# Kernel tuning notes

Measured on AMD Instinct MI355X. Metric: run time of the kernel, lower is better.

The kernel has to match this reference:

```python
import jax, jax.numpy as jnp
import numpy as np

NEG_SLOPE = 0.2


def setup_inputs() -> dict:
    key = jax.random.key(0)
    ks = jax.random.split(key, 7)
    N, E, IN, H, D = 100000, 1000000, 256, 4, 32
    feat = jax.random.normal(ks[0], (N, IN), dtype=jnp.float32)
    W_fc = jax.random.normal(ks[1], (H * D, IN), dtype=jnp.float32) * (1.0 / np.sqrt(IN))
    attn_l = jax.random.normal(ks[2], (1, H, D), dtype=jnp.float32) * 0.1
    attn_r = jax.random.normal(ks[3], (1, H, D), dtype=jnp.float32) * 0.1
    bias = jnp.zeros((H * D,), dtype=jnp.float32)
    src = jax.random.randint(ks[4], (E,), 0, N, dtype=jnp.int32)
    dst = jax.random.randint(ks[5], (E,), 0, N, dtype=jnp.int32)
    return {"feat": feat, "W_fc": W_fc, "attn_l": attn_l, "attn_r": attn_r, "bias": bias, "src": src, "dst": dst}


def reference(feat, W_fc, attn_l, attn_r, bias, src, dst):
    N = feat.shape[0]
    H, D = attn_l.shape[1], attn_l.shape[2]
    # fc projection; note: in the non-tuple path the module uses self.fc for
    # BOTH feat_src and feat_src2, so they are identical.
    h = (feat @ W_fc.T).reshape(N, H, D)  # [N,H,D]
    el = jnp.sum(h * attn_l, axis=-1)  # [N,H]
    er = jnpp_sum = jnp.sum(h * attn_r, axis=-1)  # [N,H]
    e = jax.nn.leaky_relu(el[src] + er[dst], NEG_SLOPE)  # [E,H]
    # edge softmax normalized over incoming edges of each dst node
    e_max = jax.ops.segment_max(e, dst, num_segments=N)  # [N,H]
    ex = jnp.exp(e - e_max[dst])
    denom = jax.ops.segment_sum(ex, dst, num_segments=N)  # [N,H]
    a = ex / denom[dst]  # [E,H]
    # attention-weighted aggregation: sum_e a_e * h[src_e] -> dst
    initial_ft = jax.ops.segment_sum(h[src] * a[:, :, None], dst, num_segments=N)
    # second path: u_mul_v then sum to dst (feat_src2 == feat_dst2 == h)
    add_ft = jax.ops.segment_sum(h[src] * h[dst], dst, num_segments=N)
    rst = initial_ft + add_ft + bias.reshape(1, H, D)
    return rst
```

## Files before the change

kernel.cpp:

```cpp
#include <hip/hip_runtime.h>
#include <hip/hip_bf16.h>
#include <hip/hip_fp16.h>
#include <math.h>

#define NEG_SLOPE 0.2f

typedef __attribute__((ext_vector_type(8))) short short8v;
typedef __attribute__((ext_vector_type(4))) float f32x4;

__device__ __forceinline__ float uas(unsigned int u) { return __uint_as_float(u); }

__device__ __forceinline__ unsigned short f2bf(float x) {
    __hip_bfloat16 b = __float2bfloat16(x);
    return *(unsigned short*)&b;
}

#define NPB_SHIFT 8
#define BIN_EDGES 2048
#define GEMM_EPT  4
#define BS_EPT    4
#define GEMM_BLOCKS 512

__global__ void k_prep(const float* __restrict__ W, const float* __restrict__ al,
                       const float* __restrict__ ar, short* __restrict__ wfrag,
                       int* __restrict__ bcount, int NB, int* __restrict__ tilectr) {
    int p = blockIdx.x * 256 + threadIdx.x;
    if (p < NB) bcount[p] = 0;
    if (p == 0) *tilectr = 0;
    if (p >= 144 * 32) return;
    int n = p >> 5, kg = p & 31;
    float v[8];
    if (n < 128) {
        const float* wp = W + (size_t)n * 256 + kg * 8;
        float4 v0 = *(const float4*)wp;
        float4 v1 = *(const float4*)(wp + 4);
        v[0] = v0.x; v[1] = v0.y; v[2] = v0.z; v[3] = v0.w;
        v[4] = v1.x; v[5] = v1.y; v[6] = v1.z; v[7] = v1.w;
    } else if (n < 136) {
        int i = n - 128, hh = i & 3, lr = i >> 2;
        const float* av = lr ? ar : al;
#pragma unroll
        for (int j = 0; j < 8; j++) v[j] = 0.f;
        for (int c = 0; c < 32; c++) {
            float a = av[hh * 32 + c];
            const float* wp = W + (size_t)(hh * 32 + c) * 256 + kg * 8;
#pragma unroll
            for (int j = 0; j < 8; j++) v[j] += a * wp[j];
        }
    } else {
#pragma unroll
        for (int j = 0; j < 8; j++) v[j] = 0.f;
    }
    short s8[8];
#pragma unroll
    for (int j = 0; j < 8; j++) s8[j] = (short)f2bf(v[j]);
    int kstep = kg >> 2, ntile = n >> 4;
    int L     = (kg & 3) * 16 + (n & 15);
    int slot  = kstep * 9 + ntile;
    *(short8v*)&wfrag[(slot * 64 + L) * 8] = *(short8v*)s8;
}

__global__ __launch_bounds__(512, 4) void k_gemm(const float* __restrict__ feat,
                                                 const short* __restrict__ wfrag,
                                                 unsigned short* __restrict__ hb,
                                                 float* __restrict__ el,
                                                 float* __restrict__ er, int N,
                                                 int ntiles,
                                                 int* __restrict__ tilectr,
                                                 const int* __restrict__ dst,
                                                 int* __restrict__ bcount,
                                                 int E, int NB) {
    __shared__ short wlds[36864];
    __shared__ int bh[512];
    __shared__ int tsh;
    const int t    = threadIdx.x;
    const int lane = t & 63;
    const int wave = t >> 6;
    const int g    = lane >> 4;
    const int c    = lane & 15;

#pragma unroll
    for (int i = 0; i < 9; i++) {
        int p = t + i * 512;
        *(short8v*)&wlds[(size_t)p * 8] = *(const short8v*)&wfrag[(size_t)p * 8];
    }
    __syncthreads();

    for (;;) {
        if (t == 0) tsh = atomicAdd(tilectr, 1);
        __syncthreads();
        const int tile = tsh;
        __syncthreads();
        if (tile >= ntiles) break;

        const int n0  = tile * 128;
        const int row = n0 + wave * 16 + c;
        const int rc  = row < N ? row : N - 1;
        const float* ap = feat + (size_t)rc * 256 + g * 8;

        float4 a4[16];
#pragma unroll
        for (int ks = 0; ks < 8; ks++) {
            a4[2 * ks]     = *(const float4*)(ap + ks * 32);
            a4[2 * ks + 1] = *(const float4*)(ap + ks * 32 + 4);
        }

        f32x4 acc[9];
#pragma unroll
        for (int nt = 0; nt < 9; nt++) acc[nt] = (f32x4){0.f, 0.f, 0.f, 0.f};

#pragma unroll
        for (int ks = 0; ks < 8; ks++) {
            float4 v0 = a4[2 * ks], v1 = a4[2 * ks + 1];
            short s8[8];
            s8[0] = (short)f2bf(v0.x); s8[1] = (short)f2bf(v0.y);
            s8[2] = (short)f2bf(v0.z); s8[3] = (short)f2bf(v0.w);
            s8[4] = (short)f2bf(v1.x); s8[5] = (short)f2bf(v1.y);
            s8[6] = (short)f2bf(v1.z); s8[7] = (short)f2bf(v1.w);
            short8v afrag = *(short8v*)s8;
#pragma unroll
            for (int nt = 0; nt < 9; nt++) {
                short8v b = *(short8v*)&wlds[(((size_t)ks * 9 + nt) * 64 + lane) * 8];
                acc[nt] = __builtin_amdgcn_mfma_f32_16x16x32_bf16(afrag, b, acc[nt], 0, 0, 0);
            }
        }

#pragma unroll
        for (int r = 0; r < 4; r++) {
            int m = n0 + wave * 16 + g * 4 + r;
            if (m < N) {
#pragma unroll
                for (int nt = 0; nt < 8; nt++)
                    hb[(size_t)m * 128 + nt * 16 + c] = f2bf(acc[nt][r]);
                float av = acc[8][r];
                if (c < 4)      el[(size_t)m * 4 + c]       = av;
                else if (c < 8) er[(size_t)m * 4 + (c - 4)] = av;
            }
        }
    }

    if ((size_t)blockIdx.x * BIN_EDGES < (size_t)E) {
        if (t < 512) bh[t] = 0;
        __syncthreads();
        int base = blockIdx.x * BIN_EDGES + t;
#pragma unroll
        for (int k = 0; k < GEMM_EPT; k++) {
            int idx = base + k * 512;
            if (idx < E) atomicAdd(&bh[dst[idx] >> NPB_SHIFT], 1);
        }
        __syncthreads();
        for (int i = t; i < NB; i += 512) {
            int h = bh[i];
            if (h) atomicAdd(&bcount[i], h);
        }
    }
}

__global__ __launch_bounds__(512) void k_bscan(const int* __restrict__ bcount,
                                               int* __restrict__ bbase,
                                               int* __restrict__ bcur,
                                               int* __restrict__ startA,
                                               int NB, int N) {
    __shared__ int s[512];
    int t = threadIdx.x;
    int h = (t < NB) ? bcount[t] : 0;
    s[t] = h;
    __syncthreads();
    for (int off = 1; off < 512; off <<= 1) {
        int v = (t >= off) ? s[t - off] : 0;
        __syncthreads();
        s[t] += v;
        __syncthreads();
    }
    int excl = s[t] - h;
    if (t <= NB) bbase[t] = excl;
    if (t < NB)  bcur[t]  = excl;
    if (t == 0)  startA[N] = s[511];
}

__global__ __launch_bounds__(512) void k_binscatter(const int* __restrict__ src,
                                                    const int* __restrict__ dst,
                                                    int* __restrict__ bcur,
                                                    unsigned int* __restrict__ binned,
                                                    int E, int NB) {
    __shared__ int hist[512];
    __shared__ int scn[512];
    __shared__ int lcur[512];
    __shared__ int gdelta[512];
    __shared__ int ebuf[BIN_EDGES];
    __shared__ int dbuf[BIN_EDGES];
    int t = threadIdx.x;
    hist[t] = 0;
    __syncthreads();
    int wbase = blockIdx.x * BIN_EDGES;
    int base  = wbase + t;
    int ne    = E - wbase; if (ne > BIN_EDGES) ne = BIN_EDGES;
    int sv[BS_EPT], dv[BS_EPT];
#pragma unroll
    for (int k = 0; k < BS_EPT; k++) {
        int idx = base + k * 512;
        if (idx < E) {
            sv[k] = src[idx];
            dv[k] = dst[idx];
            atomicAdd(&hist[dv[k] >> NPB_SHIFT], 1);
        } else {
            dv[k] = -1;
        }
    }
    __syncthreads();
    scn[t] = hist[t];
    __syncthreads();
    for (int off = 1; off < 512; off <<= 1) {
        int v = (t >= off) ? scn[t - off] : 0;
        __syncthreads();
        scn[t] += v;
        __syncthreads();
    }
    if (t < NB) {
        int h  = hist[t];
        int lb = scn[t] - h;
        int g  = h ? atomicAdd(&bcur[t], h) : 0;
        gdelta[t] = g - lb;
        lcur[t]   = lb;
    }
    __syncthreads();
#pragma unroll
    for (int k = 0; k < BS_EPT; k++) {
        if (dv[k] >= 0) {
            int bkt  = dv[k] >> NPB_SHIFT;
            int slot = atomicAdd(&lcur[bkt], 1);
            ebuf[slot] = sv[k];
            dbuf[slot] = dv[k];
        }
    }
    __syncthreads();
    for (int j = t; j < ne; j += 512) {
        int d = dbuf[j];
        binned[j + gdelta[d >> NPB_SHIFT]] =
            (unsigned int)ebuf[j] | ((unsigned int)(d & 255) << 24);
    }
}

__global__ __launch_bounds__(512) void k_csr(const unsigned int* __restrict__ binned,
                                             const int* __restrict__ bbase,
                                             int* __restrict__ startA,
                                             int* __restrict__ src_csr, int N) {
    __shared__ int hist[256];
    __shared__ int scn[256];
    __shared__ int cur[256];
    __shared__ int sbuf[4096];
    int b = blockIdx.x;
    int t = threadIdx.x;
    int base = bbase[b];
    int cnt  = bbase[b + 1] - base;
    int node0 = b << NPB_SHIFT;
    if (t < 256) hist[t] = 0;
    __syncthreads();
    for (int i = t; i < cnt; i += 512) {
        unsigned int e = binned[base + i];
        atomicAdd(&hist[e >> 24], 1);
    }
    __syncthreads();
    int h = (t < 256) ? hist[t] : 0;
    if (t < 256) scn[t] = h;
    __syncthreads();
    for (int off = 1; off < 256; off <<= 1) {
        int v = (t < 256 && t >= off) ? scn[t - off] : 0;
        __syncthreads();
        if (t < 256) scn[t] += v;
        __syncthreads();
    }
    if (t < 256) {
        int excl  = scn[t] - h;
        int gnode = node0 + t;
        if (gnode < N) startA[gnode] = base + excl;
        cur[t] = excl;
    }
    __syncthreads();
    if (cnt <= 4096) {
        for (int i = t; i < cnt; i += 512) {
            unsigned int e = binned[base + i];
            int p = atomicAdd(&cur[e >> 24], 1);
            sbuf[p] = (int)(e & 0xFFFFFFu);
        }
        __syncthreads();
        for (int i = t; i < cnt; i += 512)
            src_csr[base + i] = sbuf[i];
    } else {
        for (int i = t; i < cnt; i += 512) {
            unsigned int e = binned[base + i];
            int p = atomicAdd(&cur[e >> 24], 1);
            src_csr[base + p] = (int)(e & 0xFFFFFFu);
        }
    }
}

__global__ __launch_bounds__(256) void k_agg(
        const unsigned int* __restrict__ hbu,
        const float* __restrict__ el, const float* __restrict__ er,
        const int* __restrict__ src_csr, const int* __restrict__ start,
        const float* __restrict__ bias, float* __restrict__ out, int N) {
    int wid  = blockIdx.x * 4 + (threadIdx.x >> 6);
    int lane = threadIdx.x & 63;
    if (wid >= N) return;
    int beg = __builtin_amdgcn_readfirstlane(start[wid]);
    int end = __builtin_amdgcn_readfirstlane(start[wid + 1]);
    int dg  = end - beg;
    int head = lane >> 4;

    float er_own = er[(size_t)wid * 4 + head];
    unsigned int uh = hbu[(size_t)wid * 64 + lane];
    float2 bv = ((const float2*)bias)[lane];

    float S1x = 0.f, S1y = 0.f, S2x = 0.f, S2y = 0.f, dd = 0.f;
    int i = 0;
    for (; i + 8 <= dg; i += 8) {
        int b = beg + i;
        int s[8];
#pragma unroll
        for (int k = 0; k < 8; k++) s[k] = src_csr[b + k];
        unsigned int u[8];
#pragma unroll
        for (int k = 0; k < 8; k++) u[k] = hbu[(size_t)s[k] * 64 + lane];
        float ev[8];
#pragma unroll
        for (int k = 0; k < 8; k++) ev[k] = el[(size_t)s[k] * 4 + head];
#pragma unroll
        for (int k = 0; k < 8; k++) {
            float tt = ev[k] + er_own;
            tt = fmaxf(tt, NEG_SLOPE * tt);
            float w = __expf(tt);
            float x = uas(u[k] << 16), y = uas(u[k] & 0xFFFF0000u);
            S1x += x; S1y += y;
            S2x += w * x; S2y += w * y;
            dd  += w;
        }
    }
    for (; i + 4 <= dg; i += 4) {
        int b = beg + i;
        int s[4];
#pragma unroll
        for (int k = 0; k < 4; k++) s[k] = src_csr[b + k];
        unsigned int u[4];
#pragma unroll
        for (int k = 0; k < 4; k++) u[k] = hbu[(size_t)s[k] * 64 + lane];
        float ev[4];
#pragma unroll
        for (int k = 0; k < 4; k++) ev[k] = el[(size_t)s[k] * 4 + head];
#pragma unroll
        for (int k = 0; k < 4; k++) {
            float tt = ev[k] + er_own;
            tt = fmaxf(tt, NEG_SLOPE * tt);
            float w = __expf(tt);
            float x = uas(u[k] << 16), y = uas(u[k] & 0xFFFF0000u);
            S1x += x; S1y += y;
            S2x += w * x; S2y += w * y;
            dd  += w;
        }
    }
    for (; i < dg; i++) {
        int s0 = src_csr[beg + i];
        unsigned int u0 = hbu[(size_t)s0 * 64 + lane];
        float tt = el[(size_t)s0 * 4 + head] + er_own;
        tt = fmaxf(tt, NEG_SLOPE * tt);
        float w0 = __expf(tt);
        float x0 = uas(u0 << 16), y0 = uas(u0 & 0xFFFF0000u);
        S1x += x0; S1y += y0;
        S2x += w0 * x0; S2y += w0 * y0;
        dd  += w0;
    }

    float hvx = uas(uh << 16), hvy = uas(uh & 0xFFFF0000u);
    float inv = dd > 0.f ? 1.f / dd : 0.f;
    float ox = bv.x + hvx * S1x + S2x * inv;
    float oy = bv.y + hvy * S1y + S2y * inv;
    float2 o = {ox, oy};
    ((float2*)(out + (size_t)wid * 128))[lane] = o;
}

extern "C" void kernel_launch(void* const* d_in, const int* in_sizes, int n_in,
                              void* d_out, int out_size, void* d_ws, size_t ws_size,
                              hipStream_t stream) {
    const float* feat = (const float*)d_in[0];
    const float* W_fc = (const float*)d_in[1];
    const float* al   = (const float*)d_in[2];
    const float* ar   = (const float*)d_in[3];
    const float* bias = (const float*)d_in[4];
    const int*   src  = (const int*)d_in[5];
    const int*   dst  = (const int*)d_in[6];
    const int N = in_sizes[0] / 256;
    const int E = in_sizes[5];
    const int NB = (N + 255) >> NPB_SHIFT;

    char* ws = (char*)d_ws;
    size_t off = 0;
    unsigned int* hbu = (unsigned int*)(ws + off); off += (size_t)N * 64 * 4;
    float* el         = (float*)(ws + off); off += (size_t)N * 4 * 4;
    float* er         = (float*)(ws + off); off += (size_t)N * 4 * 4;
    int* startA       = (int*)(ws + off);   off += (size_t)(N + 1) * 4;
    int* src_csr      = (int*)(ws + off);   off += (size_t)E * 4;
    unsigned int* binned = (unsigned int*)(ws + off); off += (size_t)E * 4;
    short* wfrag      = (short*)(ws + off); off += (size_t)72 * 64 * 8 * 2;
    int* bcount       = (int*)(ws + off);   off += 2048;
    int* bbase        = (int*)(ws + off);   off += 2064;
    int* bcur         = (int*)(ws + off);   off += 2048;
    int* tilectr      = (int*)(ws + off);   off += 256;

    float* out = (float*)d_out;

    int ntiles = (N + 127) / 128;
    int binWG  = (E + BIN_EDGES - 1) / BIN_EDGES;
    int gemmWG = GEMM_BLOCKS > binWG ? GEMM_BLOCKS : binWG;

    k_prep<<<18, 256, 0, stream>>>(W_fc, al, ar, wfrag, bcount, NB, tilectr);
    k_gemm<<<gemmWG, 512, 0, stream>>>(feat, wfrag, (unsigned short*)hbu,
                                       el, er, N, ntiles, tilectr, dst, bcount,
                                       E, NB);
    k_bscan<<<1, 512, 0, stream>>>(bcount, bbase, bcur, startA, NB, N);
    k_binscatter<<<binWG, 512, 0, stream>>>(src, dst, bcur, binned, E, NB);
    k_csr<<<NB, 512, 0, stream>>>(binned, bbase, startA, src_csr, N);
    k_agg<<<(N + 3) / 4, 256, 0, stream>>>(hbu, el, er, src_csr, startA,
                                           bias, out, N);
}
```

Measured before the change: 272.0 us.

## Replace exact bucket counting and scan with fixed-capacity bucket slots

```diff
diff --git a/kernel.cpp b/kernel.cpp
--- a/kernel.cpp
+++ b/kernel.cpp
@@ -16,16 +16,17 @@
 }
 
 #define NPB_SHIFT 8
+#define BCAP_SHIFT 13
+#define BCAP (1 << BCAP_SHIFT)
 #define BIN_EDGES 2048
-#define GEMM_EPT  4
 #define BS_EPT    4
 #define GEMM_BLOCKS 512
 
 __global__ void k_prep(const float* __restrict__ W, const float* __restrict__ al,
                        const float* __restrict__ ar, short* __restrict__ wfrag,
-                       int* __restrict__ bcount, int NB, int* __restrict__ tilectr) {
+                       int* __restrict__ bcur, int NB, int* __restrict__ tilectr) {
     int p = blockIdx.x * 256 + threadIdx.x;
-    if (p < NB) bcount[p] = 0;
+    if (p < NB) bcur[p] = p << BCAP_SHIFT;
     if (p == 0) *tilectr = 0;
     if (p >= 144 * 32) return;
     int n = p >> 5, kg = p & 31;
@@ -66,12 +67,8 @@
                                                  float* __restrict__ el,
                                                  float* __restrict__ er, int N,
                                                  int ntiles,
-                                                 int* __restrict__ tilectr,
-                                                 const int* __restrict__ dst,
-                                                 int* __restrict__ bcount,
-                                                 int E, int NB) {
+                                                 int* __restrict__ tilectr) {
     __shared__ short wlds[36864];
-    __shared__ int bh[512];
     __shared__ int tsh;
     const int t    = threadIdx.x;
     const int lane = t & 63;
@@ -138,44 +135,6 @@
             }
         }
     }
-
-    if ((size_t)blockIdx.x * BIN_EDGES < (size_t)E) {
-        if (t < 512) bh[t] = 0;
-        __syncthreads();
-        int base = blockIdx.x * BIN_EDGES + t;
-#pragma unroll
-        for (int k = 0; k < GEMM_EPT; k++) {
-            int idx = base + k * 512;
-            if (idx < E) atomicAdd(&bh[dst[idx] >> NPB_SHIFT], 1);
-        }
-        __syncthreads();
-        for (int i = t; i < NB; i += 512) {
-            int h = bh[i];
-            if (h) atomicAdd(&bcount[i], h);
-        }
-    }
-}
-
-__global__ __launch_bounds__(512) void k_bscan(const int* __restrict__ bcount,
-                                               int* __restrict__ bbase,
-                                               int* __restrict__ bcur,
-                                               int* __restrict__ startA,
-                                               int NB, int N) {
-    __shared__ int s[512];
-    int t = threadIdx.x;
-    int h = (t < NB) ? bcount[t] : 0;
-    s[t] = h;
-    __syncthreads();
-    for (int off = 1; off < 512; off <<= 1) {
-        int v = (t >= off) ? s[t - off] : 0;
-        __syncthreads();
-        s[t] += v;
-        __syncthreads();
-    }
-    int excl = s[t] - h;
-    if (t <= NB) bbase[t] = excl;
-    if (t < NB)  bcur[t]  = excl;
-    if (t == 0)  startA[N] = s[511];
 }
 
 __global__ __launch_bounds__(512) void k_binscatter(const int* __restrict__ src,
@@ -242,8 +201,9 @@
 }
 
 __global__ __launch_bounds__(512) void k_csr(const unsigned int* __restrict__ binned,
-                                             const int* __restrict__ bbase,
+                                             const int* __restrict__ bcur,
                                              int* __restrict__ startA,
+                                             int* __restrict__ deg,
                                              int* __restrict__ src_csr, int N) {
     __shared__ int hist[256];
     __shared__ int scn[256];
@@ -251,8 +211,8 @@
     __shared__ int sbuf[4096];
     int b = blockIdx.x;
     int t = threadIdx.x;
-    int base = bbase[b];
-    int cnt  = bbase[b + 1] - base;
+    int base = b << BCAP_SHIFT;
+    int cnt  = bcur[b] - base;
     int node0 = b << NPB_SHIFT;
     if (t < 256) hist[t] = 0;
     __syncthreads();
@@ -273,7 +233,7 @@
     if (t < 256) {
         int excl  = scn[t] - h;
         int gnode = node0 + t;
-        if (gnode < N) startA[gnode] = base + excl;
+        if (gnode < N) { startA[gnode] = base + excl; deg[gnode] = h; }
         cur[t] = excl;
     }
     __syncthreads();
@@ -299,13 +259,13 @@
         const unsigned int* __restrict__ hbu,
         const float* __restrict__ el, const float* __restrict__ er,
         const int* __restrict__ src_csr, const int* __restrict__ start,
+        const int* __restrict__ deg,
         const float* __restrict__ bias, float* __restrict__ out, int N) {
     int wid  = blockIdx.x * 4 + (threadIdx.x >> 6);
     int lane = threadIdx.x & 63;
     if (wid >= N) return;
     int beg = __builtin_amdgcn_readfirstlane(start[wid]);
-    int end = __builtin_amdgcn_readfirstlane(start[wid + 1]);
-    int dg  = end - beg;
+    int dg  = __builtin_amdgcn_readfirstlane(deg[wid]);
     int head = lane >> 4;
 
     float er_own = er[(size_t)wid * 4 + head];
@@ -397,12 +357,11 @@
     unsigned int* hbu = (unsigned int*)(ws + off); off += (size_t)N * 64 * 4;
     float* el         = (float*)(ws + off); off += (size_t)N * 4 * 4;
     float* er         = (float*)(ws + off); off += (size_t)N * 4 * 4;
-    int* startA       = (int*)(ws + off);   off += (size_t)(N + 1) * 4;
-    int* src_csr      = (int*)(ws + off);   off += (size_t)E * 4;
-    unsigned int* binned = (unsigned int*)(ws + off); off += (size_t)E * 4;
+    int* startA       = (int*)(ws + off);   off += (size_t)N * 4;
+    int* deg          = (int*)(ws + off);   off += (size_t)N * 4;
+    int* src_csr      = (int*)(ws + off);   off += (size_t)NB * BCAP * 4;
+    unsigned int* binned = (unsigned int*)(ws + off); off += (size_t)NB * BCAP * 4;
     short* wfrag      = (short*)(ws + off); off += (size_t)72 * 64 * 8 * 2;
-    int* bcount       = (int*)(ws + off);   off += 2048;
-    int* bbase        = (int*)(ws + off);   off += 2064;
     int* bcur         = (int*)(ws + off);   off += 2048;
     int* tilectr      = (int*)(ws + off);   off += 256;
 
@@ -410,15 +369,12 @@
 
     int ntiles = (N + 127) / 128;
     int binWG  = (E + BIN_EDGES - 1) / BIN_EDGES;
-    int gemmWG = GEMM_BLOCKS > binWG ? GEMM_BLOCKS : binWG;
-
-    k_prep<<<18, 256, 0, stream>>>(W_fc, al, ar, wfrag, bcount, NB, tilectr);
-    k_gemm<<<gemmWG, 512, 0, stream>>>(feat, wfrag, (unsigned short*)hbu,
-                                       el, er, N, ntiles, tilectr, dst, bcount,
-                                       E, NB);
-    k_bscan<<<1, 512, 0, stream>>>(bcount, bbase, bcur, startA, NB, N);
+
+    k_prep<<<18, 256, 0, stream>>>(W_fc, al, ar, wfrag, bcur, NB, tilectr);
+    k_gemm<<<GEMM_BLOCKS, 512, 0, stream>>>(feat, wfrag, (unsigned short*)hbu,
+                                            el, er, N, ntiles, tilectr);
     k_binscatter<<<binWG, 512, 0, stream>>>(src, dst, bcur, binned, E, NB);
-    k_csr<<<NB, 512, 0, stream>>>(binned, bbase, startA, src_csr, N);
-    k_agg<<<(N + 3) / 4, 256, 0, stream>>>(hbu, el, er, src_csr, startA,
+    k_csr<<<NB, 512, 0, stream>>>(binned, bcur, startA, deg, src_csr, N);
+    k_agg<<<(N + 3) / 4, 256, 0, stream>>>(hbu, el, er, src_csr, startA, deg,
                                            bias, out, N);
 }
```

New measurement: 261.4 us. 1.04x faster.
